# Performance work log

Measured on AMD Instinct MI355X. Metric: run time of the kernel, lower is better.

## Reference

```python
import jax, jax.numpy as jnp
import numpy as np

B, P, H, D, CLASSES, L = 2048, 1024, 2048, 256, 10, 10
EP = 1e-64
LOG2PI = float(np.log(2.0 * np.pi))


def setup_inputs() -> dict:
    key = jax.random.key(0)
    ks = jax.random.split(key, 16)
    s = 0.05
    return {
        "data": jax.random.normal(ks[0], (B, P), dtype=jnp.float32),
        "mask": jax.random.randint(ks[1], (B, P), 0, 2) > 0,
        "enc_w1": jax.random.normal(ks[2], (P, H), dtype=jnp.float32) * s,
        "enc_b1": jnp.zeros((H,), jnp.float32),
        "enc_w2": jax.random.normal(ks[3], (H, 2 * D), dtype=jnp.float32) * s,
        "enc_b2": jnp.zeros((2 * D,), jnp.float32),
        "dec_w1": jax.random.normal(ks[4], (D, H), dtype=jnp.float32) * s,
        "dec_b1": jnp.zeros((H,), jnp.float32),
        "dec_w2": jax.random.normal(ks[5], (H, 3 * P), dtype=jnp.float32) * s,
        "dec_b2": jnp.zeros((3 * P,), jnp.float32),
        "cls_w1": jax.random.normal(ks[6], (P, H), dtype=jnp.float32) * s,
        "cls_b1": jnp.zeros((H,), jnp.float32),
        "cls_w2": jax.random.normal(ks[7], (H, CLASSES), dtype=jnp.float32) * s,
        "cls_b2": jnp.zeros((CLASSES,), jnp.float32),
    }


def _student_t_logprob(x, loc, scale, df):
    y = (x - loc) / scale
    return (jax.lax.lgamma((df + 1.0) * 0.5) - jax.lax.lgamma(df * 0.5)
            - 0.5 * jnp.log(df * jnp.pi) - jnp.log(scale)
            - 0.5 * (df + 1.0) * jnp.log1p(y * y / df))


def reference(data, mask, enc_w1, enc_b1, enc_w2, enc_b2,
              dec_w1, dec_b1, dec_w2, dec_b2,
              cls_w1, cls_b1, cls_w2, cls_b2):
    maskf = mask.astype(data.dtype)
    key = jax.random.key(42)
    k_eps, k_t = jax.random.split(key)

    # encoder
    he = jax.nn.relu(data @ enc_w1 + enc_b1)
    out_enc = he @ enc_w2 + enc_b2                      # [B, 2D]
    mu, sig = out_enc[:, :D], jax.nn.softplus(out_enc[:, D:]) + EP

    # reparameterized q(z|x) samples, L draws
    eps = jax.random.normal(k_eps, (L, B, D), dtype=data.dtype)
    z = mu[None] + sig[None] * eps                      # [L, B, D]
    zf = z.reshape(L * B, D)

    # decoder -> StudentT params
    hd = jax.nn.relu(zf @ dec_w1 + dec_b1)
    out_dec = hd @ dec_w2 + dec_b2                      # [L*B, 3P]
    means = out_dec[:, :P]
    scales = jax.nn.softplus(out_dec[:, P:2 * P]) + 0.001
    dfree = jax.nn.softplus(out_dec[:, 2 * P:]) + 3.0

    data_t = jnp.tile(data, (L, 1))                     # [L*B, P]
    mask_t = jnp.tile(maskf, (L, 1))
    logpx = _student_t_logprob(data_t, means, scales, dfree)
    logpxobs = jnp.sum(logpx * mask_t, axis=1).reshape(L, B)

    logpz = jnp.sum(-0.5 * z * z, axis=-1) - 0.5 * D * LOG2PI          # [L, B]
    logq = jnp.sum(-0.5 * eps * eps - jnp.log(sig)[None], axis=-1) - 0.5 * D * LOG2PI

    imp_w = jax.nn.softmax(logpxobs + logpz - logq, axis=0)            # [L, B]

    # non-reparameterized StudentT sample (torch .sample() is detached)
    t = jax.random.t(k_t, dfree, shape=dfree.shape)
    xms = jax.lax.stop_gradient(means + scales * t).reshape(L, B, P)
    xm = jnp.einsum('ki,kij->ij', imp_w, xms)

    data_imputed = jnp.where(mask, data, xm)
    hc = jax.nn.relu(data_imputed @ cls_w1 + cls_b1)
    logits = hc @ cls_w2 + cls_b2
    return (data_imputed, logits)
```

## Files before the change

### kernel.cpp

```cpp
#include <hip/hip_runtime.h>
#include <math.h>

typedef unsigned int u32;
typedef unsigned short u16;
typedef __attribute__((ext_vector_type(8))) short bf16x8;
typedef __attribute__((ext_vector_type(16))) float f32x16;

struct U2 { u32 a, b; };

__host__ __device__ __forceinline__ U2 tf2x32(u32 k0, u32 k1, u32 c0, u32 c1) {
  u32 ks2 = k0 ^ k1 ^ 0x1BD11BDAu;
  u32 x0 = c0 + k0, x1 = c1 + k1;
#define TFR(r) { x0 += x1; x1 = (x1 << (r)) | (x1 >> (32 - (r))); x1 ^= x0; }
  TFR(13) TFR(15) TFR(26) TFR(6)
  x0 += k1; x1 += ks2 + 1u;
  TFR(17) TFR(29) TFR(16) TFR(24)
  x0 += ks2; x1 += k0 + 2u;
  TFR(13) TFR(15) TFR(26) TFR(6)
  x0 += k0; x1 += k1 + 3u;
  TFR(17) TFR(29) TFR(16) TFR(24)
  x0 += k1; x1 += ks2 + 4u;
  TFR(13) TFR(15) TFR(26) TFR(6)
  x0 += ks2; x1 += k0 + 5u;
#undef TFR
  return {x0, x1};
}

__host__ __device__ __forceinline__ u32 prf32(u32 k0, u32 k1, u32 i) {
  U2 r = tf2x32(k0, k1, 0u, i);
  return r.a ^ r.b;
}

__device__ __forceinline__ float u01_from_bits(u32 bits) {
  u32 r = (bits >> 9) | 0x3f800000u;
  return __uint_as_float(r) - 1.0f;
}

__device__ __forceinline__ float erfinv_f32(float x) {
  float w = -log1pf(-x * x);
  float p;
  if (w < 5.0f) {
    w -= 2.5f;
    p = 2.81022636e-08f;
    p = fmaf(p, w, 3.43273939e-07f);
    p = fmaf(p, w, -3.5233877e-06f);
    p = fmaf(p, w, -4.39150654e-06f);
    p = fmaf(p, w, 0.00021858087f);
    p = fmaf(p, w, -0.00125372503f);
    p = fmaf(p, w, -0.00417768164f);
    p = fmaf(p, w, 0.246640727f);
    p = fmaf(p, w, 1.50140941f);
  } else {
    w = sqrtf(w) - 3.0f;
    p = -0.000200214257f;
    p = fmaf(p, w, 0.000100950558f);
    p = fmaf(p, w, 0.00134934322f);
    p = fmaf(p, w, -0.00367342844f);
    p = fmaf(p, w, 0.00573950773f);
    p = fmaf(p, w, -0.0076224613f);
    p = fmaf(p, w, 0.00943887047f);
    p = fmaf(p, w, 1.00167406f);
    p = fmaf(p, w, 2.83297682f);
  }
  return p * x;
}

__device__ __forceinline__ float normal_from_bits(u32 bits) {
  const float lo = -0.99999994f;
  float u = u01_from_bits(bits) * 2.0f + lo;
  u = fmaxf(lo, u);
  return 1.41421356237f * erfinv_f32(u);
}

__device__ __forceinline__ float softplus_f(float x) {
  return fmaxf(x, 0.0f) + log1pf(expf(-fabsf(x)));
}

__device__ float gamma_sample(u32 k0, u32 k1, float alpha) {
  U2 kk = tf2x32(k0, k1, 0u, 0u);
  k0 = kk.a; k1 = kk.b;
  float d = alpha - 0.33333334f;
  float c = 0.33333334f / sqrtf(d);
  float X, V, U;
  do {
    U2 nk = tf2x32(k0, k1, 0u, 0u);
    U2 xk = tf2x32(k0, k1, 0u, 1u);
    U2 uk = tf2x32(k0, k1, 0u, 2u);
    k0 = nk.a; k1 = nk.b;
    u32 xk0 = xk.a, xk1 = xk.b;
    float x, v;
    do {
      U2 nxt = tf2x32(xk0, xk1, 0u, 0u);
      U2 sub = tf2x32(xk0, xk1, 0u, 1u);
      xk0 = nxt.a; xk1 = nxt.b;
      x = normal_from_bits(prf32(sub.a, sub.b, 0u));
      v = 1.0f + x * c;
    } while (v <= 0.0f);
    X = x * x;
    V = (v * v) * v;
    U = u01_from_bits(prf32(uk.a, uk.b, 0u));
  } while (U >= 1.0f - 0.0331f * (X * X) &&
           logf(U) >= 0.5f * X + d * ((1.0f - V) + logf(V)));
  return d * V;
}

__device__ __forceinline__ u16 f2bf(float f) {
  u32 u = __float_as_uint(f);
  u32 r = ((u >> 16) & 1u) + 0x7fffu;
  return (u16)((u + r) >> 16);
}
__device__ __forceinline__ float bf2f(u16 h) { return __uint_as_float(((u32)h) << 16); }

__device__ __forceinline__ void split2(float v, u16& h, u16& m) {
  h = f2bf(v);
  m = f2bf(v - bf2f(h));
}

#define GLOAD16(gp, lp) __builtin_amdgcn_global_load_lds( \
    (const __attribute__((address_space(1))) void*)(gp),  \
    (__attribute__((address_space(3))) void*)(lp), 16, 0, 0)

template<bool RELU, bool SIX>
__global__ __launch_bounds__(256, 3) void gemm_s3(const u16* __restrict__ A2,
                                                  const u16* __restrict__ B2T,
                                                  const float* __restrict__ bias,
                                                  float* __restrict__ Cf,
                                                  u16* __restrict__ C2,
                                                  int N, int kbits) {
  __shared__ u16 As[128 * 64];
  __shared__ u16 Bs[128 * 64];
  const int tid = threadIdx.x;
  const int l = tid & 63, w = tid >> 6;
  const int m0 = blockIdx.y * 128, n0 = blockIdx.x * 128;
  const int K2 = 2 << kbits;
  const int srow = l >> 3;
  const int scol = ((l & 7) ^ srow) << 3;
  const u16* agr[4]; const u16* bgr[4]; u16* al[4]; u16* bl[4];
#pragma unroll
  for (int j = 0; j < 4; ++j) {
    int r = w * 32 + j * 8 + srow;
    agr[j] = A2 + (size_t)(m0 + r) * K2 + scol;
    bgr[j] = B2T + (size_t)(n0 + r) * K2 + scol;
    al[j] = &As[(w * 4 + j) * 512];
    bl[j] = &Bs[(w * 4 + j) * 512];
  }
  f32x16 acc[2][2] = {};
  const int fr = l & 31;
  const int wm = w >> 1, wn = w & 1;
  const int swz = (l & 7) << 4;
  const int hk16 = (l >> 5) << 4;
  const int nk = 3 << (kbits - 6);
  const int kmask = (1 << kbits) - 1;
  for (int kt = 0; kt < nk; ++kt) {
    int vb = kt << 6;
    int s = vb >> kbits;
    int ko = vb & kmask;
    int ao = ((s >> 1) << kbits) + ko;
    int bo = ((s & 1) << kbits) + ko;
    __syncthreads();
#pragma unroll
    for (int j = 0; j < 4; ++j) {
      GLOAD16(agr[j] + ao, al[j]);
      GLOAD16(bgr[j] + bo, bl[j]);
    }
    __syncthreads();
#pragma unroll
    for (int ks = 0; ks < 4; ++ks) {
      bf16x8 af[2], bf[2];
#pragma unroll
      for (int mi = 0; mi < 2; ++mi) {
        int ar = wm * 64 + mi * 32 + fr;
        af[mi] = *(const bf16x8*)((const char*)As + ar * 128 + ((ks * 32 + hk16) ^ swz));
      }
#pragma unroll
      for (int ni = 0; ni < 2; ++ni) {
        int br = wn * 64 + ni * 32 + fr;
        bf[ni] = *(const bf16x8*)((const char*)Bs + br * 128 + ((ks * 32 + hk16) ^ swz));
      }
#pragma unroll
      for (int mi = 0; mi < 2; ++mi)
#pragma unroll
        for (int ni = 0; ni < 2; ++ni)
          acc[mi][ni] = __builtin_amdgcn_mfma_f32_32x32x16_bf16(af[mi], bf[ni], acc[mi][ni], 0, 0, 0);
    }
  }
#pragma unroll
  for (int mi = 0; mi < 2; ++mi)
#pragma unroll
  for (int ni = 0; ni < 2; ++ni) {
    int gcol = n0 + wn * 64 + ni * 32 + fr;
    float bsv = bias[gcol];
#pragma unroll
    for (int r = 0; r < 16; ++r) {
      int grow = m0 + wm * 64 + mi * 32 + (r & 3) + 8 * (r >> 2) + 4 * (l >> 5);
      float v = acc[mi][ni][r] + bsv;
      if (RELU) v = fmaxf(v, 0.0f);
      if (!SIX) {
        Cf[(size_t)grow * N + gcol] = v;
      } else {
        u16 h, mm; split2(v, h, mm);
        u16* q = C2 + (size_t)grow * 2 * N + gcol;
        q[0] = h; q[N] = mm;
      }
    }
  }
}

__global__ __launch_bounds__(256) void k_wconv(const float* __restrict__ W, u16* __restrict__ W2T,
                                               int K, int N) {
  __shared__ float t[64][65];
  const int k0 = blockIdx.y * 64, n0 = blockIdx.x * 64;
  const int tid = threadIdx.x;
  for (int i = tid; i < 4096; i += 256) {
    int kk = i >> 6, nn = i & 63;
    t[kk][nn] = W[(size_t)(k0 + kk) * N + (n0 + nn)];
  }
  __syncthreads();
  const int nn = tid >> 2, kc = (tid & 3) << 4;
  u16* base = W2T + (size_t)(n0 + nn) * 2 * K + (k0 + kc);
#pragma unroll
  for (int kk = 0; kk < 16; ++kk) {
    u16 h, m; split2(t[kc + kk][nn], h, m);
    base[kk] = h; base[K + kk] = m;
  }
}

__global__ __launch_bounds__(256) void k_aconv(const float* __restrict__ X, u16* __restrict__ X2,
                                               int total, int kbits) {
  int i = blockIdx.x * 256 + threadIdx.x;
  if (i >= total) return;
  int K = 1 << kbits;
  int r = i >> kbits, k = i & (K - 1);
  u16 h, m; split2(X[i], h, m);
  u16* q = X2 + ((size_t)r * 2 << kbits) + k;
  q[0] = h; q[K] = m;
}

__global__ __launch_bounds__(256) void k_eps_z(const float* __restrict__ out_enc,
                                               u16* __restrict__ z2c,
                                               float* __restrict__ logpz,
                                               float* __restrict__ logq,
                                               int l0, u32 ke0, u32 ke1) {
  const int row = blockIdx.x;
  const int lb = l0 * 2048 + row;
  const int b = row & 2047;
  const int d = threadIdx.x;
  const u32 m = ((u32)lb << 8) + (u32)d;
  float mu = out_enc[b * 512 + d];
  float sg = softplus_f(out_enc[b * 512 + 256 + d]);
  float e = normal_from_bits(prf32(ke0, ke1, m));
  float zz = mu + sg * e;
  u16 h, mm; split2(zz, h, mm);
  u16* q = z2c + row * 512 + d;
  q[0] = h; q[256] = mm;
  float t1 = -0.5f * e * e - logf(sg);
  float t2 = -0.5f * zz * zz;
#pragma unroll
  for (int o = 32; o; o >>= 1) { t1 += __shfl_down(t1, o); t2 += __shfl_down(t2, o); }
  __shared__ float sm1[4], sm2[4];
  int lane = d & 63, wv = d >> 6;
  if (!lane) { sm1[wv] = t1; sm2[wv] = t2; }
  __syncthreads();
  if (d == 0) {
    float a = sm1[0] + sm1[1] + sm1[2] + sm1[3];
    float qq = sm2[0] + sm2[1] + sm2[2] + sm2[3];
    logq[lb]  = a - 235.2482645003962f;
    logpz[lb] = qq - 235.2482645003962f;
  }
}

__global__ __launch_bounds__(256) void k_logpx_xms(const float* __restrict__ odec,
                                                   const float* __restrict__ data,
                                                   const int* __restrict__ mask,
                                                   u16* __restrict__ xms,
                                                   float* __restrict__ lpxobs,
                                                   int l0, u32 kn0, u32 kn1, u32 kg0, u32 kg1) {
  const int row = blockIdx.x;
  const int lb = l0 * 2048 + row;
  const int b = row & 2047;
  const int tid = threadIdx.x;
  float lpsum = 0.0f;
  for (int j = 0; j < 4; ++j) {
    int p = tid + j * 256;
    float mean  = odec[(size_t)row * 3072 + p];
    float scale = softplus_f(odec[(size_t)row * 3072 + 1024 + p]) + 0.001f;
    float dfv   = softplus_f(odec[(size_t)row * 3072 + 2048 + p]) + 3.0f;
    u32 i = ((u32)lb << 10) + (u32)p;
    if (mask[b * 1024 + p]) {
      float x = data[b * 1024 + p];
      float y = (x - mean) / scale;
      float lp = lgammaf((dfv + 1.0f) * 0.5f) - lgammaf(dfv * 0.5f)
               - 0.5f * logf(dfv * 3.14159274f) - logf(scale)
               - 0.5f * (dfv + 1.0f) * log1pf(y * y / dfv);
      lpsum += lp;
    } else {
      float n = normal_from_bits(prf32(kn0, kn1, i));
      U2 gk = tf2x32(kg0, kg1, 0u, i);
      float half_df = dfv * 0.5f;
      float g = gamma_sample(gk.a, gk.b, half_df);
      float t = n * sqrtf(half_df / g);
      xms[i] = f2bf(mean + scale * t);
    }
  }
#pragma unroll
  for (int o = 32; o; o >>= 1) lpsum += __shfl_down(lpsum, o);
  __shared__ float sm[4];
  int lane = tid & 63, wv = tid >> 6;
  if (!lane) sm[wv] = lpsum;
  __syncthreads();
  if (tid == 0) lpxobs[lb] = sm[0] + sm[1] + sm[2] + sm[3];
}

__global__ __launch_bounds__(256) void k_impw(const float* __restrict__ lpx,
                                              const float* __restrict__ lpz,
                                              const float* __restrict__ lq,
                                              float* __restrict__ w) {
  int b = blockIdx.x * 256 + threadIdx.x;
  float s[10], mx = -INFINITY;
#pragma unroll
  for (int l = 0; l < 10; ++l) {
    s[l] = lpx[l * 2048 + b] + lpz[l * 2048 + b] - lq[l * 2048 + b];
    mx = fmaxf(mx, s[l]);
  }
  float se = 0.0f;
#pragma unroll
  for (int l = 0; l < 10; ++l) { s[l] = expf(s[l] - mx); se += s[l]; }
#pragma unroll
  for (int l = 0; l < 10; ++l) w[l * 2048 + b] = s[l] / se;
}

__global__ __launch_bounds__(256) void k_xm(const int* __restrict__ mask,
                                            const float* __restrict__ data,
                                            const float* __restrict__ impw,
                                            const u16* __restrict__ xms,
                                            u16* __restrict__ imp2,
                                            float* __restrict__ out) {
  int idx = blockIdx.x * 256 + threadIdx.x;
  int b = idx >> 10, p = idx & 1023;
  float o;
  if (mask[idx]) {
    o = data[idx];
  } else {
    float acc = 0.0f;
#pragma unroll
    for (int l = 0; l < 10; ++l)
      acc += impw[l * 2048 + b] * bf2f(xms[((size_t)l * 2048 + b) * 1024 + p]);
    o = acc;
  }
  out[idx] = o;
  u16 h, m; split2(o, h, m);
  u16* q = imp2 + (size_t)b * 2048 + p;
  q[0] = h; q[1024] = m;
}

__global__ __launch_bounds__(256) void k_cls2(const float* __restrict__ hc,
                                              const float* __restrict__ w2,
                                              const float* __restrict__ b2,
                                              float* __restrict__ out) {
  int b = blockIdx.x, tid = threadIdx.x;
  float acc[10];
#pragma unroll
  for (int c = 0; c < 10; ++c) acc[c] = 0.0f;
  for (int k = tid; k < 2048; k += 256) {
    float h = hc[(size_t)b * 2048 + k];
#pragma unroll
    for (int c = 0; c < 10; ++c) acc[c] = fmaf(h, w2[k * 10 + c], acc[c]);
  }
  __shared__ float red[4][10];
  int lane = tid & 63, wv = tid >> 6;
#pragma unroll
  for (int c = 0; c < 10; ++c) {
    float v = acc[c];
#pragma unroll
    for (int o = 32; o; o >>= 1) v += __shfl_down(v, o);
    if (!lane) red[wv][c] = v;
  }
  __syncthreads();
  if (tid < 10) out[b * 10 + tid] = red[0][tid] + red[1][tid] + red[2][tid] + red[3][tid] + b2[tid];
}

extern "C" void kernel_launch(void* const* d_in, const int* in_sizes, int n_in,
                              void* d_out, int out_size, void* d_ws, size_t ws_size,
                              hipStream_t stream) {
  const float* data   = (const float*)d_in[0];
  const int*   mask   = (const int*)d_in[1];
  const float* enc_w1 = (const float*)d_in[2];
  const float* enc_b1 = (const float*)d_in[3];
  const float* enc_w2 = (const float*)d_in[4];
  const float* enc_b2 = (const float*)d_in[5];
  const float* dec_w1 = (const float*)d_in[6];
  const float* dec_b1 = (const float*)d_in[7];
  const float* dec_w2 = (const float*)d_in[8];
  const float* dec_b2 = (const float*)d_in[9];
  const float* cls_w1 = (const float*)d_in[10];
  const float* cls_b1 = (const float*)d_in[11];
  const float* cls_w2 = (const float*)d_in[12];
  const float* cls_b2 = (const float*)d_in[13];

  float* out = (float*)d_out;
  char* wsb = (char*)d_ws;

  if (ws_size < 182779904ULL) return;

  u16*   xmsu   = (u16*)(wsb + 0);
  u16*   w_d2   = (u16*)(wsb + 41943040);
  u16*   w_d1   = (u16*)(wsb + 67108864);
  u16*   hx2    = (u16*)(wsb + 69206016);
  float* odec   = (float*)(wsb + 102760448);
  u16*   z2c    = (u16*)(wsb + 153092096);
  u16*   data2  = (u16*)(wsb + 157286400);
  u16*   w_ec   = (u16*)(wsb + 165675008);
  u16*   w_e2   = (u16*)(wsb + 174063616);
  float* logpz  = (float*)(wsb + 178257920);
  float* logq   = (float*)(wsb + 178339840);
  float* lpxobs = (float*)(wsb + 178421760);
  float* impw   = (float*)(wsb + 178503680);
  float* out_enc= (float*)(wsb + 178585600);
  float* hc     = odec;
  u16*   imp2   = data2;

  U2 ke = tf2x32(0u, 42u, 0u, 0u);
  U2 kt = tf2x32(0u, 42u, 0u, 1u);
  U2 kn = tf2x32(kt.a, kt.b, 0u, 0u);
  U2 kg = tf2x32(kt.a, kt.b, 0u, 1u);

  dim3 blk(256);
  k_aconv<<<8192, blk, 0, stream>>>(data, data2, 2097152, 10);
  k_wconv<<<dim3(32, 16), blk, 0, stream>>>(enc_w1, w_ec, 1024, 2048);
  k_wconv<<<dim3(8, 32),  blk, 0, stream>>>(enc_w2, w_e2, 2048, 512);
  k_wconv<<<dim3(48, 32), blk, 0, stream>>>(dec_w2, w_d2, 2048, 3072);
  k_wconv<<<dim3(32, 4),  blk, 0, stream>>>(dec_w1, w_d1, 256, 2048);

  gemm_s3<true,  true ><<<dim3(16, 16), blk, 0, stream>>>(data2, w_ec, enc_b1, nullptr, hx2, 2048, 10);
  gemm_s3<false, false><<<dim3(4, 16),  blk, 0, stream>>>(hx2, w_e2, enc_b2, out_enc, nullptr, 512, 11);

  for (int l0 = 0; l0 < 10; l0 += 2) {
    k_eps_z<<<4096, blk, 0, stream>>>(out_enc, z2c, logpz, logq, l0, ke.a, ke.b);
    gemm_s3<true,  true ><<<dim3(16, 32), blk, 0, stream>>>(z2c, w_d1, dec_b1, nullptr, hx2, 2048, 8);
    gemm_s3<false, false><<<dim3(24, 32), blk, 0, stream>>>(hx2, w_d2, dec_b2, odec, nullptr, 3072, 11);
    k_logpx_xms<<<4096, blk, 0, stream>>>(odec, data, mask, xmsu, lpxobs, l0, kn.a, kn.b, kg.a, kg.b);
  }

  k_impw<<<8, blk, 0, stream>>>(lpxobs, logpz, logq, impw);
  k_xm<<<8192, blk, 0, stream>>>(mask, data, impw, xmsu, imp2, out);

  k_wconv<<<dim3(32, 16), blk, 0, stream>>>(cls_w1, w_ec, 1024, 2048);
  gemm_s3<true, false><<<dim3(16, 16), blk, 0, stream>>>(imp2, w_ec, cls_b1, hc, nullptr, 2048, 10);
  k_cls2<<<2048, blk, 0, stream>>>(hc, cls_w2, cls_b2, out + 2048 * 1024);
}
```

Baseline: 2.136 ms.

## Split logpx and Student-T sampling into separate kernels with compacted missing-index lists

The fused per-row kernel, which either scores observed entries or draws Student-T samples for missing ones, becomes two kernels. A new prepass builds a compacted list of missing positions per batch row using a prefix scan. The sampling kernel then iterates only over those positions, so the costly threefry and gamma sampling path no longer diverges within wavefronts against the lgamma path. The cost is an extra launch per chunk, a second read of odec, and scattered gathers through the index list.

```diff
diff --git a/kernel.cpp b/kernel.cpp
--- a/kernel.cpp
+++ b/kernel.cpp
@@ -236,6 +236,34 @@
   q[0] = h; q[K] = m;
 }
 
+__global__ __launch_bounds__(256) void k_build(const int* __restrict__ mask,
+                                               u16* __restrict__ miss,
+                                               int* __restrict__ nmiss) {
+  const int b = blockIdx.x, tid = threadIdx.x;
+  const int* mrow = mask + b * 1024;
+  const int pb = tid * 4;
+  int m0 = (mrow[pb] == 0), m1 = (mrow[pb + 1] == 0),
+      m2 = (mrow[pb + 2] == 0), m3 = (mrow[pb + 3] == 0);
+  int cnt = m0 + m1 + m2 + m3;
+  __shared__ int sc[256];
+  sc[tid] = cnt;
+  __syncthreads();
+  for (int off = 1; off < 256; off <<= 1) {
+    int v = 0;
+    if (tid >= off) v = sc[tid - off];
+    __syncthreads();
+    sc[tid] += v;
+    __syncthreads();
+  }
+  int pos = sc[tid] - cnt;
+  u16* mr = miss + b * 1024;
+  if (m0) mr[pos++] = (u16)pb;
+  if (m1) mr[pos++] = (u16)(pb + 1);
+  if (m2) mr[pos++] = (u16)(pb + 2);
+  if (m3) mr[pos++] = (u16)(pb + 3);
+  if (tid == 255) nmiss[b] = sc[255];
+}
+
 __global__ __launch_bounds__(256) void k_eps_z(const float* __restrict__ out_enc,
                                                u16* __restrict__ z2c,
                                                float* __restrict__ logpz,
@@ -269,12 +297,11 @@
   }
 }
 
-__global__ __launch_bounds__(256) void k_logpx_xms(const float* __restrict__ odec,
-                                                   const float* __restrict__ data,
-                                                   const int* __restrict__ mask,
-                                                   u16* __restrict__ xms,
-                                                   float* __restrict__ lpxobs,
-                                                   int l0, u32 kn0, u32 kn1, u32 kg0, u32 kg1) {
+__global__ __launch_bounds__(256) void k_lpx(const float* __restrict__ odec,
+                                             const float* __restrict__ data,
+                                             const int* __restrict__ mask,
+                                             float* __restrict__ lpxobs,
+                                             int l0) {
   const int row = blockIdx.x;
   const int lb = l0 * 2048 + row;
   const int b = row & 2047;
@@ -282,24 +309,16 @@
   float lpsum = 0.0f;
   for (int j = 0; j < 4; ++j) {
     int p = tid + j * 256;
-    float mean  = odec[(size_t)row * 3072 + p];
-    float scale = softplus_f(odec[(size_t)row * 3072 + 1024 + p]) + 0.001f;
-    float dfv   = softplus_f(odec[(size_t)row * 3072 + 2048 + p]) + 3.0f;
-    u32 i = ((u32)lb << 10) + (u32)p;
     if (mask[b * 1024 + p]) {
+      float mean  = odec[(size_t)row * 3072 + p];
+      float scale = softplus_f(odec[(size_t)row * 3072 + 1024 + p]) + 0.001f;
+      float dfv   = softplus_f(odec[(size_t)row * 3072 + 2048 + p]) + 3.0f;
       float x = data[b * 1024 + p];
       float y = (x - mean) / scale;
       float lp = lgammaf((dfv + 1.0f) * 0.5f) - lgammaf(dfv * 0.5f)
                - 0.5f * logf(dfv * 3.14159274f) - logf(scale)
                - 0.5f * (dfv + 1.0f) * log1pf(y * y / dfv);
       lpsum += lp;
-    } else {
-      float n = normal_from_bits(prf32(kn0, kn1, i));
-      U2 gk = tf2x32(kg0, kg1, 0u, i);
-      float half_df = dfv * 0.5f;
-      float g = gamma_sample(gk.a, gk.b, half_df);
-      float t = n * sqrtf(half_df / g);
-      xms[i] = f2bf(mean + scale * t);
     }
   }
 #pragma unroll
@@ -309,6 +328,31 @@
   if (!lane) sm[wv] = lpsum;
   __syncthreads();
   if (tid == 0) lpxobs[lb] = sm[0] + sm[1] + sm[2] + sm[3];
+}
+
+__global__ __launch_bounds__(256) void k_sample(const float* __restrict__ odec,
+                                                const u16* __restrict__ miss,
+                                                const int* __restrict__ nmiss,
+                                                u16* __restrict__ xms,
+                                                int l0, u32 kn0, u32 kn1, u32 kg0, u32 kg1) {
+  const int row = blockIdx.x;
+  const int lb = l0 * 2048 + row;
+  const int b = row & 2047;
+  const int nm = nmiss[b];
+  const u16* mr = miss + b * 1024;
+  for (int t = threadIdx.x; t < nm; t += 256) {
+    int p = mr[t];
+    float mean  = odec[(size_t)row * 3072 + p];
+    float scale = softplus_f(odec[(size_t)row * 3072 + 1024 + p]) + 0.001f;
+    float dfv   = softplus_f(odec[(size_t)row * 3072 + 2048 + p]) + 3.0f;
+    u32 i = ((u32)lb << 10) + (u32)p;
+    float n = normal_from_bits(prf32(kn0, kn1, i));
+    U2 gk = tf2x32(kg0, kg1, 0u, i);
+    float half_df = dfv * 0.5f;
+    float g = gamma_sample(gk.a, gk.b, half_df);
+    float tt = n * sqrtf(half_df / g);
+    xms[i] = f2bf(mean + scale * tt);
+  }
 }
 
 __global__ __launch_bounds__(256) void k_impw(const float* __restrict__ lpx,
@@ -400,7 +444,7 @@
   float* out = (float*)d_out;
   char* wsb = (char*)d_ws;
 
-  if (ws_size < 182779904ULL) return;
+  if (ws_size < 186982400ULL) return;
 
   u16*   xmsu   = (u16*)(wsb + 0);
   u16*   w_d2   = (u16*)(wsb + 41943040);
@@ -416,6 +460,8 @@
   float* lpxobs = (float*)(wsb + 178421760);
   float* impw   = (float*)(wsb + 178503680);
   float* out_enc= (float*)(wsb + 178585600);
+  u16*   miss   = (u16*)(wsb + 182779904);
+  int*   nmiss  = (int*)(wsb + 186974208);
   float* hc     = odec;
   u16*   imp2   = data2;
 
@@ -430,6 +476,7 @@
   k_wconv<<<dim3(8, 32),  blk, 0, stream>>>(enc_w2, w_e2, 2048, 512);
   k_wconv<<<dim3(48, 32), blk, 0, stream>>>(dec_w2, w_d2, 2048, 3072);
   k_wconv<<<dim3(32, 4),  blk, 0, stream>>>(dec_w1, w_d1, 256, 2048);
+  k_build<<<2048, blk, 0, stream>>>(mask, miss, nmiss);
 
   gemm_s3<true,  true ><<<dim3(16, 16), blk, 0, stream>>>(data2, w_ec, enc_b1, nullptr, hx2, 2048, 10);
   gemm_s3<false, false><<<dim3(4, 16),  blk, 0, stream>>>(hx2, w_e2, enc_b2, out_enc, nullptr, 512, 11);
@@ -438,7 +485,8 @@
     k_eps_z<<<4096, blk, 0, stream>>>(out_enc, z2c, logpz, logq, l0, ke.a, ke.b);
     gemm_s3<true,  true ><<<dim3(16, 32), blk, 0, stream>>>(z2c, w_d1, dec_b1, nullptr, hx2, 2048, 8);
     gemm_s3<false, false><<<dim3(24, 32), blk, 0, stream>>>(hx2, w_d2, dec_b2, odec, nullptr, 3072, 11);
-    k_logpx_xms<<<4096, blk, 0, stream>>>(odec, data, mask, xmsu, lpxobs, l0, kn.a, kn.b, kg.a, kg.b);
+    k_lpx<<<4096, blk, 0, stream>>>(odec, data, mask, lpxobs, l0);
+    k_sample<<<4096, blk, 0, stream>>>(odec, miss, nmiss, xmsu, l0, kn.a, kn.b, kg.a, kg.b);
   }
 
   k_impw<<<8, blk, 0, stream>>>(lpxobs, logpz, logq, impw);
```

Result: faster. 1.985 ms (-7.0%).
